# Kernel optimization log

Hardware: AMD Instinct MI355X
Metric: run time of the kernel (lower is better)

The kernel has to match this reference:

```python
import jax, jax.numpy as jnp
import numpy as np

B, S, DIM = 2, 2048, 2048
NH, NKV = 16, 8
HD = DIM // NH  # 128
ROPE_THETA = 10000.0


def setup_inputs() -> dict:
    key = jax.random.key(0)
    ks = jax.random.split(key, 7)
    std = DIM ** -0.5
    x = jax.random.normal(ks[0], (B, S, DIM), jnp.float32)
    wq = jax.random.normal(ks[1], (NH * HD, DIM), jnp.float32) * std
    wk = jax.random.normal(ks[2], (NKV * HD, DIM), jnp.float32) * std
    wv = jax.random.normal(ks[3], (NKV * HD, DIM), jnp.float32) * std
    wo = jax.random.normal(ks[4], (DIM, NH * HD), jnp.float32) * std
    inv_freq = 1.0 / (ROPE_THETA ** (jnp.arange(0, HD, 2, dtype=jnp.float32) / HD))
    ang = jnp.arange(S, dtype=jnp.float32)[:, None] * inv_freq[None, :]  # [S, HD//2]
    freqs_cos = jnp.cos(ang)
    freqs_sin = jnp.sin(ang)
    # diffusion-style random per-batch token mask: t ~ U[0,1) per batch row
    t = jax.random.uniform(ks[5], (B, 1))
    mask = jax.random.uniform(ks[6], (B, S)) < t  # True = masked key
    mask = mask.at[:, 0].set(False)  # first token never masked
    return dict(x=x, wq=wq, wk=wk, wv=wv, wo=wo,
                freqs_cos=freqs_cos, freqs_sin=freqs_sin, mask=mask)


def _rope(x, cos, sin):
    # x: [b, s, h, d]; pairs (x[2i], x[2i+1]) rotated by angle[s, i]
    xr, xi = x[..., 0::2], x[..., 1::2]
    c = cos[None, :, None, :]
    s = sin[None, :, None, :]
    out = jnp.stack([xr * c - xi * s, xr * s + xi * c], axis=-1)
    return out.reshape(x.shape)


def reference(x, wq, wk, wv, wo, freqs_cos, freqs_sin, mask):
    b, s, _ = x.shape
    xq = jnp.einsum('bsd,ed->bse', x, wq).reshape(b, s, NH, HD)
    xk = jnp.einsum('bsd,ed->bse', x, wk).reshape(b, s, NKV, HD)
    xv = jnp.einsum('bsd,ed->bse', x, wv).reshape(b, s, NKV, HD)
    xq = _rope(xq, freqs_cos, freqs_sin)
    xk = _rope(xk, freqs_cos, freqs_sin)
    n_rep = NH // NKV
    xk = jnp.repeat(xk, n_rep, axis=2)  # repeat_kv (GQA)
    xv = jnp.repeat(xv, n_rep, axis=2)
    q = xq.transpose(0, 2, 1, 3)  # [b, h, s, d]
    k = xk.transpose(0, 2, 1, 3)
    v = xv.transpose(0, 2, 1, 3)
    scale = 1.0 / np.sqrt(HD).astype(np.float32)
    scores = jnp.einsum('bhqd,bhkd->bhqk', q, k) * scale  # [b, h, s, s]
    scores = jnp.where(mask[:, None, None, :], -jnp.inf, scores)
    probs = jax.nn.softmax(scores, axis=-1)
    out = jnp.einsum('bhqk,bhkd->bhqd', probs, v)
    out = out.transpose(0, 2, 1, 3).reshape(b, s, NH * HD)
    return jnp.einsum('bse,de->bsd', out, wo)
```

## Files before the change

### kernel.cpp

```cpp
#include <hip/hip_runtime.h>
#include <hip/hip_bf16.h>
#include <cstdint>
#include <cstddef>

#define S_LEN   2048
#define NHQ     16
#define NKV_H   8
#define HD_DIM  128
#define DMODEL  2048
#define BATCH   2
#define KVD     (NKV_H * HD_DIM)
#define QKV_LD  4096

typedef float f32x4  __attribute__((ext_vector_type(4)));
typedef __bf16 bf16x8 __attribute__((ext_vector_type(8)));
typedef __bf16 bf16x4 __attribute__((ext_vector_type(4)));

__device__ __forceinline__ void gload_lds16(const __bf16* g, __bf16* l) {
    __builtin_amdgcn_global_load_lds(
        (const __attribute__((address_space(1))) void*)g,
        (__attribute__((address_space(3))) void*)l, 16, 0, 0);
}

__global__ __launch_bounds__(256)
void prep_kernel(const unsigned* __restrict__ x, int* __restrict__ flag_x,
                 const unsigned* __restrict__ fc, int* __restrict__ flag_fc,
                 const unsigned char* __restrict__ mraw,
                 unsigned char* __restrict__ mout, int n) {
    if (blockIdx.x == 0) {
        __shared__ int cnt;
        if (threadIdx.x == 0) cnt = 0;
        __syncthreads();
        int c = 0;
        for (int j = threadIdx.x; j < 1024; j += 256) {
            unsigned hw = x[j] & 0xFFFFu;
            unsigned e  = (hw >> 7) & 0xFF;
            if (hw == 0u || (e >= 118 && e <= 132)) c++;
        }
        atomicAdd(&cnt, c);
        __syncthreads();
        if (threadIdx.x == 0) *flag_x = (cnt > 512) ? 1 : 0;
    } else if (blockIdx.x == 1) {
        if (threadIdx.x == 0) *flag_fc = (fc[0] == 0x3F803F80u) ? 1 : 0;
    } else {
        __shared__ int f_bf16, f_f32, f_u8;
        if (threadIdx.x == 0) { f_bf16 = 0; f_f32 = 0; f_u8 = 0; }
        __syncthreads();
        const unsigned* dw = (const unsigned*)mraw;
        int ndw = n / 4;
        for (int j = threadIdx.x; j < ndw; j += blockDim.x) {
            unsigned v = dw[j];
            if (v == 0x00003F80u || v == 0x3F803F80u) f_bf16 = 1;
            else if (v == 0x3F800000u) f_f32 = 1;
            else if (v & 0xFFFFFFFEu) f_u8 = 1;
        }
        __syncthreads();
        int layout;
        if (f_bf16) layout = 3;
        else if (f_f32) layout = 2;
        else if (f_u8) layout = 0;
        else layout = 1;
        for (int i = threadIdx.x; i < n; i += blockDim.x) {
            unsigned v;
            if (layout == 0)      v = mraw[i];
            else if (layout == 3) v = ((const unsigned short*)mraw)[i];
            else                  v = ((const unsigned*)mraw)[i];
            mout[i] = v ? 1u : 0u;
        }
    }
}

__device__ __forceinline__ void conv8(const void* src, __bf16* dst,
                                      size_t off, int isbf16) {
    if (isbf16) {
        *reinterpret_cast<uint4*>(dst + off) =
            *reinterpret_cast<const uint4*>((const __bf16*)src + off);
    } else {
        const float* f = (const float*)src + off;
        float4 a = *reinterpret_cast<const float4*>(f);
        float4 b = *reinterpret_cast<const float4*>(f + 4);
        bf16x8 v;
        v[0] = (__bf16)a.x; v[1] = (__bf16)a.y; v[2] = (__bf16)a.z; v[3] = (__bf16)a.w;
        v[4] = (__bf16)b.x; v[5] = (__bf16)b.y; v[6] = (__bf16)b.z; v[7] = (__bf16)b.w;
        *reinterpret_cast<bf16x8*>(dst + off) = v;
    }
}

__global__ __launch_bounds__(256)
void conv_all_kernel(const void* __restrict__ x,  const void* __restrict__ wq,
                     const void* __restrict__ wk, const void* __restrict__ wv,
                     __bf16* __restrict__ xb, __bf16* __restrict__ wcomb,
                     const int* __restrict__ dflag) {
    int i = blockIdx.x * 256 + threadIdx.x;
    int isb = *dflag;
    if (i < 1048576) {
        conv8(x, xb, (size_t)i * 8, isb);
    } else if (i < 1572864) {
        conv8(wq, wcomb, (size_t)(i - 1048576) * 8, isb);
    } else if (i < 1835008) {
        conv8(wk, wcomb + (size_t)2048 * 2048, (size_t)(i - 1572864) * 8, isb);
    } else {
        conv8(wv, wcomb + (size_t)3072 * 2048, (size_t)(i - 1835008) * 8, isb);
    }
}

__global__ __launch_bounds__(256)
void conv_bf16_strided_kernel(const void* __restrict__ src,
                              __bf16* __restrict__ dstbase,
                              int n8, const int* __restrict__ dflag) {
    int i = blockIdx.x * blockDim.x + threadIdx.x;
    if (i >= n8) return;
    size_t off = (size_t)i * 8;
    size_t row = off >> 11;
    size_t col = off & 2047;
    __bf16* dst = dstbase + row * QKV_LD + col;
    if (*dflag) {
        *reinterpret_cast<uint4*>(dst) =
            *reinterpret_cast<const uint4*>((const __bf16*)src + off);
    } else {
        const float* f = (const float*)src + off;
        float4 a = *reinterpret_cast<const float4*>(f);
        float4 b = *reinterpret_cast<const float4*>(f + 4);
        bf16x8 v;
        v[0] = (__bf16)a.x; v[1] = (__bf16)a.y; v[2] = (__bf16)a.z; v[3] = (__bf16)a.w;
        v[4] = (__bf16)b.x; v[5] = (__bf16)b.y; v[6] = (__bf16)b.z; v[7] = (__bf16)b.w;
        *reinterpret_cast<bf16x8*>(dst) = v;
    }
}

template <bool OUT_BF16>
__global__ __launch_bounds__(256)
void gemm_bt_async(const __bf16* __restrict__ A, const __bf16* __restrict__ Bw,
                   void* __restrict__ Cv, int K, int lda, int ldb, int ldc) {
    __shared__ __align__(16) __bf16 As[128 * 64];
    __shared__ __align__(16) __bf16 Bs[128 * 64];

    const int t    = threadIdx.x;
    const int w    = t >> 6;
    const int lane = t & 63;
    const int quad = lane >> 4;
    const int l16  = lane & 15;
    const int wm   = (w >> 1) * 64;
    const int wn   = (w & 1) * 64;

    const int nwg  = gridDim.x * gridDim.y;
    const int lin  = blockIdx.y * gridDim.x + blockIdx.x;
    const int swz  = (lin & 7) * (nwg >> 3) + (lin >> 3);
    const int m0   = (swz % gridDim.x) * 128;
    const int n0   = (swz / gridDim.x) * 128;

    const int rl   = lane >> 3;
    const int gl   = lane & 7;

    f32x4 acc[4][4];
#pragma unroll
    for (int i = 0; i < 4; ++i)
#pragma unroll
        for (int j = 0; j < 4; ++j) acc[i][j] = (f32x4){0.f, 0.f, 0.f, 0.f};

    for (int k0 = 0; k0 < K; k0 += 64) {
        __syncthreads();
#pragma unroll
        for (int p = 0; p < 4; ++p) {
            const int rowb = w * 32 + p * 8;
            const int r    = rowb + rl;
            const int gA   = gl ^ rl;
            gload_lds16(A  + (size_t)(m0 + r) * lda + k0 + gA * 8, &As[rowb * 64]);
            gload_lds16(Bw + (size_t)(n0 + r) * ldb + k0 + gA * 8, &Bs[rowb * 64]);
        }
        __syncthreads();
#pragma unroll
        for (int ks = 0; ks < 2; ++ks) {
            const int G = ks * 4 + quad;
            const int gsw = (G ^ (l16 & 7)) * 8;
            bf16x8 af[4], bf[4];
#pragma unroll
            for (int i = 0; i < 4; ++i)
                af[i] = *reinterpret_cast<const bf16x8*>(
                    &As[(wm + i * 16 + l16) * 64 + gsw]);
#pragma unroll
            for (int j = 0; j < 4; ++j)
                bf[j] = *reinterpret_cast<const bf16x8*>(
                    &Bs[(wn + j * 16 + l16) * 64 + gsw]);
#pragma unroll
            for (int i = 0; i < 4; ++i)
#pragma unroll
                for (int j = 0; j < 4; ++j)
                    acc[i][j] = __builtin_amdgcn_mfma_f32_16x16x32_bf16(
                        af[i], bf[j], acc[i][j], 0, 0, 0);
        }
    }
#pragma unroll
    for (int i = 0; i < 4; ++i)
#pragma unroll
        for (int r = 0; r < 4; ++r) {
            size_t m = (size_t)(m0 + wm + i * 16 + quad * 4 + r);
#pragma unroll
            for (int j = 0; j < 4; ++j) {
                int n = n0 + wn + j * 16 + l16;
                if constexpr (OUT_BF16)
                    ((__hip_bfloat16*)Cv)[m * ldc + n] = __float2bfloat16(acc[i][j][r]);
                else
                    ((float*)Cv)[m * ldc + n] = acc[i][j][r];
            }
        }
}

__global__ void rope_kernel(__hip_bfloat16* __restrict__ xqk,
                            const void* __restrict__ cosv,
                            const void* __restrict__ sinv,
                            const int* __restrict__ dflag_fc,
                            int npairs) {
    int idx = blockIdx.x * blockDim.x + threadIdx.x;
    if (idx >= npairs) return;
    int i  = idx & 63;
    int h  = (idx >> 6) % 24;
    int bs = idx / (64 * 24);
    int s  = bs & (S_LEN - 1);
    float c, sn;
    if (*dflag_fc) {
        c  = __bfloat162float(((const __hip_bfloat16*)cosv)[s * 64 + i]);
        sn = __bfloat162float(((const __hip_bfloat16*)sinv)[s * 64 + i]);
    } else {
        c  = ((const float*)cosv)[s * 64 + i];
        sn = ((const float*)sinv)[s * 64 + i];
    }
    unsigned* p = (unsigned*)(xqk + (size_t)bs * QKV_LD + h * HD_DIM) + i;
    unsigned u = *p;
    float xr = __uint_as_float(u << 16);
    float xi = __uint_as_float(u & 0xFFFF0000u);
    float o0 = xr * c - xi * sn;
    float o1 = xr * sn + xi * c;
    union { __hip_bfloat16 h2[2]; unsigned u32; } out;
    out.h2[0] = __float2bfloat16(o0);
    out.h2[1] = __float2bfloat16(o1);
    *p = out.u32;
}

__global__ __launch_bounds__(256)
void transpose_v_kernel(const __hip_bfloat16* __restrict__ xv,
                        __hip_bfloat16* __restrict__ vt) {
    __shared__ unsigned short T[32][36];
    const int t  = threadIdx.x;
    const int s0 = blockIdx.x * 32;
    const int d0 = blockIdx.y * 32;
    const int z  = blockIdx.z;
    const int b  = z >> 3;
    const int kv = z & 7;
    {
        int sr = t >> 3, dc = (t & 7) * 4;
        const unsigned short* p = (const unsigned short*)xv
            + (size_t)(b * S_LEN + s0 + sr) * QKV_LD + kv * 128 + d0 + dc;
        uint2 v = *reinterpret_cast<const uint2*>(p);
        T[sr][dc + 0] = (unsigned short)(v.x & 0xFFFFu);
        T[sr][dc + 1] = (unsigned short)(v.x >> 16);
        T[sr][dc + 2] = (unsigned short)(v.y & 0xFFFFu);
        T[sr][dc + 3] = (unsigned short)(v.y >> 16);
    }
    __syncthreads();
    {
        int dr = t >> 3, sc = (t & 7) * 4;
        unsigned w0 = (unsigned)T[sc + 0][dr] | ((unsigned)T[sc + 1][dr] << 16);
        unsigned w1 = (unsigned)T[sc + 2][dr] | ((unsigned)T[sc + 3][dr] << 16);
        unsigned short* q = (unsigned short*)vt
            + ((size_t)z * 128 + d0 + dr) * S_LEN + s0 + sc;
        uint2 v; v.x = w0; v.y = w1;
        *reinterpret_cast<uint2*>(q) = v;
    }
}

__global__ __launch_bounds__(256)
void attn_mfma2_kernel(__hip_bfloat16* qkv,
                       const __hip_bfloat16* __restrict__ vt_g,
                       const unsigned char* __restrict__ msk) {
    __shared__ __align__(16) __bf16 Ks[2][64 * 128];
    __shared__ __align__(16) __bf16 Vt[2][128 * 64];
    __shared__ __align__(16) __bf16 Ps[4][16][64];

    const int t    = threadIdx.x;
    const int w    = t >> 6;
    const int lane = t & 63;
    const int quad = lane >> 4;
    const int l16  = lane & 15;

    const int bid = ((blockIdx.x & 7) << 7) | (blockIdx.x >> 3);
    const int qt  = bid & 31;
    const int h   = (bid >> 5) & (NHQ - 1);
    const int b   = bid >> 9;
    const int kvh = h >> 1;
    const int q0  = qt * 64;

    bf16x8 qf[4];
    {
        const __bf16* qrow = (const __bf16*)qkv
            + (size_t)(b * S_LEN + q0 + w * 16 + l16) * QKV_LD + h * 128 + quad * 8;
#pragma unroll
        for (int ks = 0; ks < 4; ++ks)
            qf[ks] = *reinterpret_cast<const bf16x8*>(qrow + ks * 32);
    }

    float m_r = -INFINITY, l_r = 0.f;
    f32x4 o[8];
#pragma unroll
    for (int d0 = 0; d0 < 8; ++d0) o[d0] = (f32x4){0.f, 0.f, 0.f, 0.f};

    const float scale2 = 0.08838834764831845f * 1.4426950408889634f;
    const int gbase = lane & 48;

    const __bf16* kp[4];
    const __bf16* vp[4];
    {
        const __bf16* xk = (const __bf16*)qkv + 2048;
        const int krl = lane >> 4, kgl = lane & 15;
        const int vrl = lane >> 3, vgl = lane & 7;
#pragma unroll
        for (int p = 0; p < 4; ++p) {
            const int row = w * 16 + p * 4 + krl;
            kp[p] = xk + (size_t)(b * S_LEN + row) * QKV_LD
                       + kvh * 128 + (kgl ^ (row & 7)) * 8;
        }
#pragma unroll
        for (int p = 0; p < 4; ++p) {
            const int row = w * 32 + p * 8 + vrl;
            vp[p] = (const __bf16*)vt_g
                  + ((size_t)(b * NKV_H + kvh) * 128 + row) * S_LEN
                  + (vgl ^ (row & 7)) * 8;
        }
    }
    const unsigned char* mbase = msk + b * S_LEN;

    f32x4 scA[4], scB[4];
    unsigned mkA[4], mkB[4];

#define STAGE_K(SB) { _Pragma("unroll") \
    for (int p_ = 0; p_ < 4; ++p_) { \
        gload_lds16(kp[p_], &Ks[SB][(w * 16 + p_ * 4) * 128]); \
        kp[p_] += 64 * QKV_LD; } }

#define STAGE_V(SB) { _Pragma("unroll") \
    for (int p_ = 0; p_ < 4; ++p_) { \
        gload_lds16(vp[p_], &Vt[SB][(w * 32 + p_ * 8) * 64]); \
        vp[p_] += 64; } }

#define LOAD_MK(MK, K0) { \
    const unsigned* mp_ = (const unsigned*)(mbase + (K0)); \
    _Pragma("unroll") for (int n_ = 0; n_ < 4; ++n_) MK[n_] = mp_[n_ * 4 + quad]; }

#define QKT(CB, SC) { \
    _Pragma("unroll") for (int n_ = 0; n_ < 4; ++n_) SC[n_] = (f32x4){0.f, 0.f, 0.f, 0.f}; \
    _Pragma("unroll") for (int ks_ = 0; ks_ < 4; ++ks_) { \
        const int G_ = ks_ * 4 + quad; \
        _Pragma("unroll") for (int n_ = 0; n_ < 4; ++n_) { \
            const int row_  = n_ * 16 + l16; \
            const int slot_ = G_ ^ (row_ & 7); \
            bf16x8 kf_ = *reinterpret_cast<const bf16x8*>(&Ks[CB][row_ * 128 + slot_ * 8]); \
            SC[n_] = __builtin_amdgcn_mfma_f32_16x16x32_bf16(kf_, qf[ks_], SC[n_], 0, 0, 0); } } }

#define SMPV(SC, MK, CB) { \
    _Pragma("unroll") for (int n_ = 0; n_ < 4; ++n_) \
        _Pragma("unroll") for (int r_ = 0; r_ < 4; ++r_) \
            SC[n_][r_] = ((MK[n_] >> (r_ * 8)) & 0xFF) ? -INFINITY : SC[n_][r_]; \
    float tq_[4]; \
    _Pragma("unroll") for (int n_ = 0; n_ < 4; ++n_) \
        tq_[n_] = fmaxf(fmaxf(SC[n_][0], SC[n_][1]), fmaxf(SC[n_][2], SC[n_][3])); \
    float rm_ = fmaxf(fmaxf(tq_[0], tq_[1]), fmaxf(tq_[2], tq_[3])); \
    rm_ = fmaxf(rm_, __shfl_xor(rm_, 16, 64)); \
    rm_ = fmaxf(rm_, __shfl_xor(rm_, 32, 64)); \
    bool need_ = (rm_ - m_r) * scale2 > 8.0f; \
    if (__any((int)need_)) { \
        float mn_ = fmaxf(m_r, rm_); \
        float al_ = exp2f((m_r - mn_) * scale2); \
        m_r = mn_; l_r *= al_; \
        float alq_[4]; \
        _Pragma("unroll") for (int r_ = 0; r_ < 4; ++r_) \
            alq_[r_] = __shfl(al_, gbase | (quad * 4 + r_), 64); \
        _Pragma("unroll") for (int d_ = 0; d_ < 8; ++d_) \
            _Pragma("unroll") for (int r_ = 0; r_ < 4; ++r_) o[d_][r_] *= alq_[r_]; } \
    float negm_ = -m_r * scale2; \
    _Pragma("unroll") for (int n_ = 0; n_ < 4; ++n_) { \
        _Pragma("unroll") for (int r_ = 0; r_ < 4; ++r_) { \
            float p_ = exp2f(fmaf(SC[n_][r_], scale2, negm_)); \
            SC[n_][r_] = p_; l_r += p_; } \
        const int kb_    = n_ * 16 + quad * 4; \
        const int gran_  = kb_ >> 3; \
        const int half4_ = kb_ & 4; \
        const int slot_  = gran_ ^ (l16 & 7); \
        bf16x4 pk_; \
        pk_[0] = (__bf16)SC[n_][0]; pk_[1] = (__bf16)SC[n_][1]; \
        pk_[2] = (__bf16)SC[n_][2]; pk_[3] = (__bf16)SC[n_][3]; \
        *reinterpret_cast<bf16x4*>(&Ps[w][l16][slot_ * 8 + half4_]) = pk_; } \
    __builtin_amdgcn_s_setprio(1); \
    _Pragma("unroll") for (int kk_ = 0; kk_ < 64; kk_ += 32) { \
        const int Gp_    = (kk_ >> 3) + quad; \
        const int slotp_ = Gp_ ^ (l16 & 7); \
        bf16x8 af_ = *reinterpret_cast<const bf16x8*>(&Ps[w][l16][slotp_ * 8]); \
        _Pragma("unroll") for (int d_ = 0; d_ < 8; ++d_) { \
            const int row_  = d_ * 16 + l16; \
            const int slot_ = Gp_ ^ (row_ & 7); \
            bf16x8 bf_ = *reinterpret_cast<const bf16x8*>(&Vt[CB][row_ * 64 + slot_ * 8]); \
            o[d_] = __builtin_amdgcn_mfma_f32_16x16x32_bf16(af_, bf_, o[d_], 0, 0, 0); } } \
    __builtin_amdgcn_s_setprio(0); }

    STAGE_K(0);
    __syncthreads();

    STAGE_K(1);
    STAGE_V(0);
    LOAD_MK(mkA, 0);
    QKT(0, scA);
    __syncthreads();

    for (int it = 0; it < 15; ++it) {
        const int k0 = it * 128 + 64;
        STAGE_K(0);
        STAGE_V(1);
        LOAD_MK(mkB, k0);
        QKT(1, scB);
        SMPV(scA, mkA, 0);
        __syncthreads();
        STAGE_K(1);
        STAGE_V(0);
        LOAD_MK(mkA, k0 + 64);
        QKT(0, scA);
        SMPV(scB, mkB, 1);
        __syncthreads();
    }

    STAGE_V(1);
    LOAD_MK(mkB, 1984);
    QKT(1, scB);
    SMPV(scA, mkA, 0);
    __syncthreads();

    SMPV(scB, mkB, 1);

#undef STAGE_K
#undef STAGE_V
#undef LOAD_MK
#undef QKT
#undef SMPV

    float ls = l_r;
    ls += __shfl_xor(ls, 16, 64);
    ls += __shfl_xor(ls, 32, 64);
    float invl = 1.f / ls;
    float invq[4];
#pragma unroll
    for (int r = 0; r < 4; ++r)
        invq[r] = __shfl(invl, gbase | (quad * 4 + r), 64);
    __hip_bfloat16* att = qkv;
#pragma unroll
    for (int d0 = 0; d0 < 8; ++d0)
#pragma unroll
        for (int r = 0; r < 4; ++r) {
            size_t row = (size_t)(b * S_LEN + q0 + w * 16 + quad * 4 + r);
            att[row * QKV_LD + h * 128 + d0 * 16 + l16] =
                __float2bfloat16(o[d0][r] * invq[r]);
        }
}

extern "C" void kernel_launch(void* const* d_in, const int* in_sizes, int n_in,
                              void* d_out, int out_size, void* d_ws, size_t ws_size,
                              hipStream_t stream) {
    const void* x  = d_in[0];
    const void* wq = d_in[1];
    const void* wk = d_in[2];
    const void* wv = d_in[3];
    const void* wo = d_in[4];
    const void* fc = d_in[5];
    const void* fs = d_in[6];
    const unsigned char* mraw = (const unsigned char*)d_in[7];

    const int M = BATCH * S_LEN;
    char* wsb = (char*)d_ws;
    int* dflag_x  = (int*)wsb;
    int* dflag_fc = (int*)(wsb + 64);
    unsigned char* mnorm = (unsigned char*)(wsb + 128);
    __hip_bfloat16* qkv = (__hip_bfloat16*)(wsb + 8192);

    char* dob = (char*)d_out;
    __bf16* xb    = (__bf16*)dob;
    __bf16* wcomb = (__bf16*)(dob + (16u << 20));
    __hip_bfloat16* vt = (__hip_bfloat16*)d_out;

    hipLaunchKernelGGL(prep_kernel, dim3(3), dim3(256), 0, stream,
                       (const unsigned*)x, dflag_x, (const unsigned*)fc, dflag_fc,
                       mraw, mnorm, BATCH * S_LEN);

    hipLaunchKernelGGL(conv_all_kernel, dim3(8192), dim3(256), 0, stream,
                       x, wq, wk, wv, xb, wcomb, dflag_x);

    hipLaunchKernelGGL((gemm_bt_async<true>), dim3(M / 128, QKV_LD / 128), dim3(256), 0, stream,
                       xb, wcomb, (void*)qkv, DMODEL, DMODEL, DMODEL, QKV_LD);

    int npairs = M * 24 * (HD_DIM / 2);
    hipLaunchKernelGGL(rope_kernel, dim3(npairs / 256), dim3(256), 0, stream,
                       qkv, fc, fs, dflag_fc, npairs);

    hipLaunchKernelGGL(transpose_v_kernel, dim3(S_LEN / 32, HD_DIM / 32, BATCH * NKV_H),
                       dim3(256), 0, stream, qkv + 3072, vt);

    hipLaunchKernelGGL(attn_mfma2_kernel, dim3(BATCH * NHQ * (S_LEN / 64)), dim3(256), 0, stream,
                       qkv, vt, mnorm);

    hipLaunchKernelGGL(conv_bf16_strided_kernel, dim3((DMODEL * DMODEL / 8) / 256), dim3(256), 0, stream,
                       wo, (__bf16*)qkv + 2048, DMODEL * DMODEL / 8, dflag_x);

    hipLaunchKernelGGL((gemm_bt_async<false>), dim3(M / 128, DMODEL / 128), dim3(256), 0, stream,
                       (const __bf16*)qkv, (const __bf16*)qkv + 2048, d_out,
                       DMODEL, QKV_LD, QKV_LD, DMODEL);
}
```

Before: 426.8 us.

## Fuse RoPE into QKV GEMM epilogue and fold prep into conversion kernel

Applies the rotary embedding inside the QKV GEMM epilogue, using a lane shuffle to fetch the paired element, and removes the separate rope kernel. This saves a read-modify-write pass over Q and K. The prep kernel is also dropped: its dtype-sniffing is now done per block inside the conversion kernels, and the mask normalisation and freq-flag work move into extra blocks of conv_all. Fewer launches and less memory traffic come at the cost of redundant sniffing work in every block and more epilogue loads for cos/sin.

```diff
diff --git a/kernel.cpp b/kernel.cpp
--- a/kernel.cpp
+++ b/kernel.cpp
@@ -22,52 +22,18 @@
         (__attribute__((address_space(3))) void*)l, 16, 0, 0);
 }
 
-__global__ __launch_bounds__(256)
-void prep_kernel(const unsigned* __restrict__ x, int* __restrict__ flag_x,
-                 const unsigned* __restrict__ fc, int* __restrict__ flag_fc,
-                 const unsigned char* __restrict__ mraw,
-                 unsigned char* __restrict__ mout, int n) {
-    if (blockIdx.x == 0) {
-        __shared__ int cnt;
-        if (threadIdx.x == 0) cnt = 0;
-        __syncthreads();
-        int c = 0;
-        for (int j = threadIdx.x; j < 1024; j += 256) {
-            unsigned hw = x[j] & 0xFFFFu;
-            unsigned e  = (hw >> 7) & 0xFF;
-            if (hw == 0u || (e >= 118 && e <= 132)) c++;
-        }
-        atomicAdd(&cnt, c);
-        __syncthreads();
-        if (threadIdx.x == 0) *flag_x = (cnt > 512) ? 1 : 0;
-    } else if (blockIdx.x == 1) {
-        if (threadIdx.x == 0) *flag_fc = (fc[0] == 0x3F803F80u) ? 1 : 0;
-    } else {
-        __shared__ int f_bf16, f_f32, f_u8;
-        if (threadIdx.x == 0) { f_bf16 = 0; f_f32 = 0; f_u8 = 0; }
-        __syncthreads();
-        const unsigned* dw = (const unsigned*)mraw;
-        int ndw = n / 4;
-        for (int j = threadIdx.x; j < ndw; j += blockDim.x) {
-            unsigned v = dw[j];
-            if (v == 0x00003F80u || v == 0x3F803F80u) f_bf16 = 1;
-            else if (v == 0x3F800000u) f_f32 = 1;
-            else if (v & 0xFFFFFFFEu) f_u8 = 1;
-        }
-        __syncthreads();
-        int layout;
-        if (f_bf16) layout = 3;
-        else if (f_f32) layout = 2;
-        else if (f_u8) layout = 0;
-        else layout = 1;
-        for (int i = threadIdx.x; i < n; i += blockDim.x) {
-            unsigned v;
-            if (layout == 0)      v = mraw[i];
-            else if (layout == 3) v = ((const unsigned short*)mraw)[i];
-            else                  v = ((const unsigned*)mraw)[i];
-            mout[i] = v ? 1u : 0u;
-        }
-    }
+__device__ __forceinline__ int sniff_bf16(const unsigned* buf, int* cntp) {
+    if (threadIdx.x == 0) *cntp = 0;
+    __syncthreads();
+    int c = 0;
+    for (int j = threadIdx.x; j < 1024; j += 256) {
+        unsigned hw = buf[j] & 0xFFFFu;
+        unsigned e  = (hw >> 7) & 0xFF;
+        if (hw == 0u || (e >= 118 && e <= 132)) c++;
+    }
+    atomicAdd(cntp, c);
+    __syncthreads();
+    return *cntp > 512;
 }
 
 __device__ __forceinline__ void conv8(const void* src, __bf16* dst,
@@ -90,9 +56,43 @@
 void conv_all_kernel(const void* __restrict__ x,  const void* __restrict__ wq,
                      const void* __restrict__ wk, const void* __restrict__ wv,
                      __bf16* __restrict__ xb, __bf16* __restrict__ wcomb,
-                     const int* __restrict__ dflag) {
+                     const unsigned* __restrict__ fc, int* __restrict__ dflag_fc,
+                     const unsigned char* __restrict__ mraw,
+                     unsigned char* __restrict__ mout, int nmask) {
+    __shared__ int sh[4];
+    if (blockIdx.x == 8192) {
+        if (threadIdx.x == 0) *dflag_fc = (fc[0] == 0x3F803F80u) ? 1 : 0;
+        return;
+    }
+    if (blockIdx.x == 8193) {
+        __shared__ int f_bf16, f_f32, f_u8;
+        if (threadIdx.x == 0) { f_bf16 = 0; f_f32 = 0; f_u8 = 0; }
+        __syncthreads();
+        const unsigned* dw = (const unsigned*)mraw;
+        int ndw = nmask / 4;
+        for (int j = threadIdx.x; j < ndw; j += blockDim.x) {
+            unsigned v = dw[j];
+            if (v == 0x00003F80u || v == 0x3F803F80u) f_bf16 = 1;
+            else if (v == 0x3F800000u) f_f32 = 1;
+            else if (v & 0xFFFFFFFEu) f_u8 = 1;
+        }
+        __syncthreads();
+        int layout;
+        if (f_bf16) layout = 3;
+        else if (f_f32) layout = 2;
+        else if (f_u8) layout = 0;
+        else layout = 1;
+        for (int i = threadIdx.x; i < nmask; i += blockDim.x) {
+            unsigned v;
+            if (layout == 0)      v = mraw[i];
+            else if (layout == 3) v = ((const unsigned short*)mraw)[i];
+            else                  v = ((const unsigned*)mraw)[i];
+            mout[i] = v ? 1u : 0u;
+        }
+        return;
+    }
+    int isb = sniff_bf16((const unsigned*)x, &sh[0]);
     int i = blockIdx.x * 256 + threadIdx.x;
-    int isb = *dflag;
     if (i < 1048576) {
         conv8(x, xb, (size_t)i * 8, isb);
     } else if (i < 1572864) {
@@ -106,15 +106,16 @@
 
 __global__ __launch_bounds__(256)
 void conv_bf16_strided_kernel(const void* __restrict__ src,
-                              __bf16* __restrict__ dstbase,
-                              int n8, const int* __restrict__ dflag) {
+                              __bf16* __restrict__ dstbase, int n8) {
+    __shared__ int cnt;
+    int isb = sniff_bf16((const unsigned*)src, &cnt);
     int i = blockIdx.x * blockDim.x + threadIdx.x;
     if (i >= n8) return;
     size_t off = (size_t)i * 8;
     size_t row = off >> 11;
     size_t col = off & 2047;
     __bf16* dst = dstbase + row * QKV_LD + col;
-    if (*dflag) {
+    if (isb) {
         *reinterpret_cast<uint4*>(dst) =
             *reinterpret_cast<const uint4*>((const __bf16*)src + off);
     } else {
@@ -128,10 +129,12 @@
     }
 }
 
-template <bool OUT_BF16>
+template <bool OUT_BF16, bool ROPE>
 __global__ __launch_bounds__(256)
 void gemm_bt_async(const __bf16* __restrict__ A, const __bf16* __restrict__ Bw,
-                   void* __restrict__ Cv, int K, int lda, int ldb, int ldc) {
+                   void* __restrict__ Cv, int K, int lda, int ldb, int ldc,
+                   const void* __restrict__ cosv, const void* __restrict__ sinv,
+                   const int* __restrict__ dflag_fc) {
     __shared__ __align__(16) __bf16 As[128 * 64];
     __shared__ __align__(16) __bf16 Bs[128 * 64];
 
@@ -190,51 +193,39 @@
                         af[i], bf[j], acc[i][j], 0, 0, 0);
         }
     }
+
+    bool fcb = false;
+    if constexpr (ROPE) fcb = (*dflag_fc != 0);
 #pragma unroll
     for (int i = 0; i < 4; ++i)
 #pragma unroll
         for (int r = 0; r < 4; ++r) {
             size_t m = (size_t)(m0 + wm + i * 16 + quad * 4 + r);
+            const int spos = (int)(m & (S_LEN - 1));
 #pragma unroll
             for (int j = 0; j < 4; ++j) {
                 int n = n0 + wn + j * 16 + l16;
+                float v = acc[i][j][r];
+                if (ROPE && (n0 + wn + j * 16 < 3072)) {
+                    int pair = (n & 127) >> 1;
+                    float c, s;
+                    if (fcb) {
+                        c = __bfloat162float(((const __hip_bfloat16*)cosv)[spos * 64 + pair]);
+                        s = __bfloat162float(((const __hip_bfloat16*)sinv)[spos * 64 + pair]);
+                    } else {
+                        c = ((const float*)cosv)[spos * 64 + pair];
+                        s = ((const float*)sinv)[spos * 64 + pair];
+                    }
+                    float partner = __shfl_xor(v, 1, 64);
+                    float ssgn = (n & 1) ? s : -s;
+                    v = fmaf(v, c, partner * ssgn);
+                }
                 if constexpr (OUT_BF16)
-                    ((__hip_bfloat16*)Cv)[m * ldc + n] = __float2bfloat16(acc[i][j][r]);
+                    ((__hip_bfloat16*)Cv)[m * ldc + n] = __float2bfloat16(v);
                 else
-                    ((float*)Cv)[m * ldc + n] = acc[i][j][r];
+                    ((float*)Cv)[m * ldc + n] = v;
             }
         }
-}
-
-__global__ void rope_kernel(__hip_bfloat16* __restrict__ xqk,
-                            const void* __restrict__ cosv,
-                            const void* __restrict__ sinv,
-                            const int* __restrict__ dflag_fc,
-                            int npairs) {
-    int idx = blockIdx.x * blockDim.x + threadIdx.x;
-    if (idx >= npairs) return;
-    int i  = idx & 63;
-    int h  = (idx >> 6) % 24;
-    int bs = idx / (64 * 24);
-    int s  = bs & (S_LEN - 1);
-    float c, sn;
-    if (*dflag_fc) {
-        c  = __bfloat162float(((const __hip_bfloat16*)cosv)[s * 64 + i]);
-        sn = __bfloat162float(((const __hip_bfloat16*)sinv)[s * 64 + i]);
-    } else {
-        c  = ((const float*)cosv)[s * 64 + i];
-        sn = ((const float*)sinv)[s * 64 + i];
-    }
-    unsigned* p = (unsigned*)(xqk + (size_t)bs * QKV_LD + h * HD_DIM) + i;
-    unsigned u = *p;
-    float xr = __uint_as_float(u << 16);
-    float xi = __uint_as_float(u & 0xFFFF0000u);
-    float o0 = xr * c - xi * sn;
-    float o1 = xr * sn + xi * c;
-    union { __hip_bfloat16 h2[2]; unsigned u32; } out;
-    out.h2[0] = __float2bfloat16(o0);
-    out.h2[1] = __float2bfloat16(o1);
-    *p = out.u32;
 }
 
 __global__ __launch_bounds__(256)
@@ -473,7 +464,6 @@
 
     const int M = BATCH * S_LEN;
     char* wsb = (char*)d_ws;
-    int* dflag_x  = (int*)wsb;
     int* dflag_fc = (int*)(wsb + 64);
     unsigned char* mnorm = (unsigned char*)(wsb + 128);
     __hip_bfloat16* qkv = (__hip_bfloat16*)(wsb + 8192);
@@ -483,19 +473,13 @@
     __bf16* wcomb = (__bf16*)(dob + (16u << 20));
     __hip_bfloat16* vt = (__hip_bfloat16*)d_out;
 
-    hipLaunchKernelGGL(prep_kernel, dim3(3), dim3(256), 0, stream,
-                       (const unsigned*)x, dflag_x, (const unsigned*)fc, dflag_fc,
-                       mraw, mnorm, BATCH * S_LEN);
-
-    hipLaunchKernelGGL(conv_all_kernel, dim3(8192), dim3(256), 0, stream,
-                       x, wq, wk, wv, xb, wcomb, dflag_x);
-
-    hipLaunchKernelGGL((gemm_bt_async<true>), dim3(M / 128, QKV_LD / 128), dim3(256), 0, stream,
-                       xb, wcomb, (void*)qkv, DMODEL, DMODEL, DMODEL, QKV_LD);
-
-    int npairs = M * 24 * (HD_DIM / 2);
-    hipLaunchKernelGGL(rope_kernel, dim3(npairs / 256), dim3(256), 0, stream,
-                       qkv, fc, fs, dflag_fc, npairs);
+    hipLaunchKernelGGL(conv_all_kernel, dim3(8194), dim3(256), 0, stream,
+                       x, wq, wk, wv, xb, wcomb,
+                       (const unsigned*)fc, dflag_fc, mraw, mnorm, BATCH * S_LEN);
+
+    hipLaunchKernelGGL((gemm_bt_async<true, true>), dim3(M / 128, QKV_LD / 128), dim3(256), 0, stream,
+                       xb, wcomb, (void*)qkv, DMODEL, DMODEL, DMODEL, QKV_LD,
+                       fc, fs, dflag_fc);
 
     hipLaunchKernelGGL(transpose_v_kernel, dim3(S_LEN / 32, HD_DIM / 32, BATCH * NKV_H),
                        dim3(256), 0, stream, qkv + 3072, vt);
@@ -504,9 +488,10 @@
                        qkv, vt, mnorm);
 
     hipLaunchKernelGGL(conv_bf16_strided_kernel, dim3((DMODEL * DMODEL / 8) / 256), dim3(256), 0, stream,
-                       wo, (__bf16*)qkv + 2048, DMODEL * DMODEL / 8, dflag_x);
-
-    hipLaunchKernelGGL((gemm_bt_async<false>), dim3(M / 128, DMODEL / 128), dim3(256), 0, stream,
+                       wo, (__bf16*)qkv + 2048, DMODEL * DMODEL / 8);
+
+    hipLaunchKernelGGL((gemm_bt_async<false, false>), dim3(M / 128, DMODEL / 128), dim3(256), 0, stream,
                        (const __bf16*)qkv, (const __bf16*)qkv + 2048, d_out,
-                       DMODEL, QKV_LD, QKV_LD, DMODEL);
-}
+                       DMODEL, QKV_LD, QKV_LD, DMODEL,
+                       nullptr, nullptr, nullptr);
+}
```

Result: slower. 440.2 us (+3.1%).
